# Performance work log

Hardware: AMD Instinct MI355X
Metric: run time of the kernel (lower is better)

## Reference

```python
import jax, jax.numpy as jnp
import numpy as np

SW, FB, EMB, H = 96, 64, 512, 3   # seg_width, freq_bandwidth, embedding_dim, num_heads
B, T = 4, 1024
F = SW * FB


def setup_inputs() -> dict:
    key = jax.random.key(0)
    ks = jax.random.split(key, 12)
    s = 0.02
    dh = SW // H
    return {
        "x": jax.random.normal(ks[0], (B, T, F), jnp.float32),
        "o_enc": jax.random.randint(ks[1], (B, T), 0, 2, jnp.int32),
        "r_enc": jax.random.normal(ks[2], (B, T, EMB), jnp.float32),
        "Wq": jax.random.normal(ks[3], (SW, SW), jnp.float32) * s,
        "bq": jnp.zeros((SW,), jnp.float32),
        "Wk": jax.random.normal(ks[4], (SW, SW), jnp.float32) * s,
        "bk": jnp.zeros((SW,), jnp.float32),
        "Wv": jax.random.normal(ks[5], (SW, SW), jnp.float32) * s,
        "bv": jnp.zeros((SW,), jnp.float32),
        "Er": jax.random.normal(ks[6], (FB, dh), jnp.float32) * s,   # relative pos embeddings, max_len = FB
        "W1": jax.random.normal(ks[7], (SW, 4 * SW), jnp.float32) * s,
        "b1": jnp.zeros((4 * SW,), jnp.float32),
        "W2": jax.random.normal(ks[8], (4 * SW, SW), jnp.float32) * s,
        "b2": jnp.zeros((SW,), jnp.float32),
        "We": jax.random.normal(ks[9], (F, EMB), jnp.float32) * s,
        "be": jnp.zeros((EMB,), jnp.float32),
    }


def _skew(qer):
    # qer: (N, h, L, L) -> Srel via Music-Transformer skewing
    padded = jnp.pad(qer, ((0, 0), (0, 0), (0, 0), (1, 0)))      # (N,h,L,L+1)
    n, h, l, l1 = padded.shape
    return padded.reshape(n, h, l1, l)[:, :, 1:, :]               # (N,h,L,L)


def _rel_attention(x, Wq, bq, Wk, bk, Wv, bv, Er):
    # x: (N, L, D); relative global self-attention with causal mask
    N, L, D = x.shape
    dh = D // H

    def heads(t):
        return t.reshape(N, L, H, dh).transpose(0, 2, 1, 3)       # (N,h,L,dh)

    q = heads(x @ Wq + bq)
    k = heads(x @ Wk + bk)
    v = heads(x @ Wv + bv)
    qer = jnp.einsum('nhld,md->nhlm', q, Er)                      # (N,h,L,L)
    srel = _skew(qer)
    scores = (jnp.einsum('nhld,nhmd->nhlm', q, k) + srel) / jnp.sqrt(jnp.asarray(dh, x.dtype))
    causal = jnp.triu(jnp.ones((L, L), bool), 1)
    scores = jnp.where(causal, jnp.finfo(scores.dtype).min, scores)
    attn = jax.nn.softmax(scores, axis=-1)
    out = jnp.einsum('nhlm,nhmd->nhld', attn, v)
    return out.transpose(0, 2, 1, 3).reshape(N, L, D)


def _segmentwise_mean(data, block_ids):
    # data: (B,T,E), block_ids: (B,T) contiguous non-decreasing segment ids in [0,T)
    Bn, Tn, En = data.shape
    seg_sum = jax.vmap(lambda d, i: jax.ops.segment_sum(d, i, num_segments=Tn))(data, block_ids)
    cnt = jax.vmap(lambda i: jax.ops.segment_sum(jnp.ones_like(i), i, num_segments=Tn))(block_ids)
    means = seg_sum / jnp.maximum(cnt, 1).astype(data.dtype)[..., None]
    is_start = jnp.concatenate(
        [jnp.ones((Bn, 1), bool), block_ids[:, 1:] != block_ids[:, :-1]], axis=1)
    gathered = jnp.take_along_axis(means, block_ids[..., None], axis=1)   # (B,T,E)
    # original writes each block's mean only at the block's first position, zeros elsewhere
    return jnp.where(is_start[..., None], gathered, jnp.zeros((), data.dtype))


def reference(x, o_enc, r_enc, Wq, bq, Wk, bk, Wv, bv, Er, W1, b1, W2, b2, We, be):
    Bn, Tn, Fn = x.shape
    xr = x.reshape(Bn * Tn, SW, FB).transpose(0, 2, 1)            # (B*T, FB, SW)
    emb = _rel_attention(xr, Wq, bq, Wk, bk, Wv, bv, Er)
    emb = jax.nn.relu(emb @ W1 + b1) @ W2 + b2                    # FFN: SW -> 4SW -> SW
    emb = emb.transpose(0, 2, 1).reshape(Bn, Tn, Fn)
    emb = emb @ We + be                                           # (B,T,EMB)
    # nn.LayerNorm(emb.shape): normalize over the WHOLE tensor, no affine, eps=1e-8
    mu = emb.mean()
    var = ((emb - mu) ** 2).mean()
    emb = (emb - mu) / jnp.sqrt(var + 1e-8)
    # _regionalize: block ids from cumsum of binary boundary indicators
    block_ids = jnp.cumsum(o_enc, axis=1)
    block_ids = block_ids - block_ids[:, :1]                      # matches 'if b[0]==1: b -= 1'
    block_means = _segmentwise_mean(emb, block_ids)
    return block_means + r_enc + emb
```

## Files before the change

kernel.cpp:

```cpp
#include <hip/hip_runtime.h>
#include <hip/hip_bf16.h>


typedef __attribute__((ext_vector_type(8))) short bf16x8;
typedef __attribute__((ext_vector_type(4))) float f32x4;

struct PtrTab { const void* p[16]; };

enum : int {
  O_WQT = 0,
  O_BQ  = 9984,
  O_WKT = 10080,
  O_BK  = 20064,
  O_WVT = 20160,
  O_BV  = 30144,
  O_ER  = 30240,
  O_W1T = 32288,
  O_B1  = 72224,
  O_W2C = 72608,
  O_B2  = 118688,
  O_WET = 118784
};

__device__ __forceinline__ float b2f(__hip_bfloat16 v) { return __bfloat162float(v); }
__device__ __forceinline__ __hip_bfloat16 f2b(float v) { return __float2bfloat16(v); }

__global__ __launch_bounds__(256) void prep_kernel(PtrTab tab,
                                                   __hip_bfloat16* __restrict__ Wc,
                                                   float* __restrict__ sums)
{
    __shared__ __hip_bfloat16 tile[64][65];
    const int bid = blockIdx.x, tid = threadIdx.x;
    const int kt = bid % 96, nt = bid / 96;
    const float* We = (const float*)tab.p[14];
    const int k0 = kt * 64, n0 = nt * 64;
    for (int e = tid; e < 4096; e += 256) {
        int kk = e >> 6, nn = e & 63;
        tile[nn][kk] = f2b(We[(size_t)(k0 + kk) * 512 + n0 + nn]);
    }
    __syncthreads();
    __hip_bfloat16* dstT = Wc + O_WET + ((size_t)nt * 96 + kt) * 4096;
    for (int e = tid; e < 4096; e += 256) dstT[e] = tile[e >> 6][e & 63];

    const int g = bid * 256 + tid;
    const int stride = gridDim.x * 256;
    const float* Wq = (const float*)tab.p[3];
    const float* bq = (const float*)tab.p[4];
    const float* Wk = (const float*)tab.p[5];
    const float* bk = (const float*)tab.p[6];
    const float* Wv = (const float*)tab.p[7];
    const float* bv = (const float*)tab.p[8];
    const float* Er = (const float*)tab.p[9];
    const float* W1 = (const float*)tab.p[10];
    const float* b1 = (const float*)tab.p[11];
    const float* W2 = (const float*)tab.p[12];
    const float* b2 = (const float*)tab.p[13];

    for (int t = 0; t < 3; ++t) {
        const float* W = (t == 0 ? Wq : t == 1 ? Wk : Wv);
        __hip_bfloat16* d = Wc + t * 10080;
        for (int i = g; i < 9984; i += stride) {
            int j = i / 104, c = i - j * 104;
            d[i] = (c < 96) ? f2b(W[c * 96 + j]) : f2b(0.0f);
        }
    }
    for (int i = g; i < 96; i += stride) {
        Wc[O_BQ + i] = f2b(bq[i]);
        Wc[O_BK + i] = f2b(bk[i]);
        Wc[O_BV + i] = f2b(bv[i]);
        Wc[O_B2 + i] = f2b(b2[i]);
    }
    for (int i = g; i < 2048; i += stride) Wc[O_ER + i] = f2b(Er[i]);
    for (int i = g; i < 39936; i += stride) {
        int j = i / 104, c = i - j * 104;
        Wc[O_W1T + i] = (c < 96) ? f2b(W1[c * 384 + j]) : f2b(0.0f);
    }
    for (int i = g; i < 384; i += stride) Wc[O_B1 + i] = f2b(b1[i]);
    for (int i = g; i < 46080; i += stride) {
        int kc = i / 3840, r = i - kc * 3840;
        int nn = r / 40, kk = r - nn * 40;
        Wc[O_W2C + i] = (kk < 32) ? f2b(W2[(kc * 32 + kk) * 96 + nn]) : f2b(0.0f);
    }
    if (g < 2) sums[g] = 0.f;
}

__global__ __launch_bounds__(256) void attn_ffn_kernel(
    const float* __restrict__ x, const __hip_bfloat16* __restrict__ Wc,
    __hip_bfloat16* __restrict__ M)
{
    const int n = blockIdx.x, tid = threadIdx.x;
    const int w = tid >> 6, lane = tid & 63, quad = lane >> 4, ln = lane & 15;

    __shared__ __align__(16) char smem[50432];
    __hip_bfloat16* xs  = (__hip_bfloat16*)(smem);
    __hip_bfloat16* wb  = (__hip_bfloat16*)(smem + 13312);
    __hip_bfloat16* PB  = (__hip_bfloat16*)(smem + 13312);
    __hip_bfloat16* kS  = (__hip_bfloat16*)(smem + 23296);
    __hip_bfloat16* vT  = (__hip_bfloat16*)(smem + 36608);
    __hip_bfloat16* hid = (__hip_bfloat16*)(smem + 23296);

    const f32x4 z4 = {0.f, 0.f, 0.f, 0.f};
    const int rowb = 16 * w + quad * 4;

    bf16x8 wf[9], wfn[9];
    #pragma unroll
    for (int i = 0; i < 9; ++i)
        wf[i] = *(const bf16x8*)(Wc + O_WQT + ((i % 3) * 16 + ln) * 104 + (i / 3) * 32 + quad * 8);

    {
        const float* xb = x + (size_t)n * 6144;
        const int sb = w * 24;
        for (int c = 0; c < 3; ++c) {
            float v[8];
            #pragma unroll
            for (int j = 0; j < 8; ++j) v[j] = xb[(sb + c * 8 + j) * 64 + lane];
            union { __hip_bfloat16 h[8]; bf16x8 v8; } pk;
            #pragma unroll
            for (int j = 0; j < 8; ++j) pk.h[j] = f2b(v[j]);
            *(bf16x8*)(xs + lane * 104 + sb + c * 8) = pk.v8;
        }
    }
    __syncthreads();

    bf16x8 aqr[3];

    for (int st = 0; st < 6; ++st) {
        const int t = st >> 1, half = st & 1;
        if (st < 5) {
            const __hip_bfloat16* nb = Wc + ((st + 1) >> 1) * 10080 + ((st + 1) & 1) * 4992;
            #pragma unroll
            for (int i = 0; i < 9; ++i)
                wfn[i] = *(const bf16x8*)(nb + ((i % 3) * 16 + ln) * 104 + (i / 3) * 32 + quad * 8);
        }
        f32x4 acc[3] = {z4, z4, z4};
        #pragma unroll
        for (int ks = 0; ks < 3; ++ks) {
            bf16x8 a = *(const bf16x8*)(xs + (16 * w + ln) * 104 + ks * 32 + quad * 8);
            #pragma unroll
            for (int ct = 0; ct < 3; ++ct)
                acc[ct] = __builtin_amdgcn_mfma_f32_16x16x32_bf16(a, wf[ks * 3 + ct], acc[ct], 0, 0, 0);
        }
        const int j0 = half * 48;
        const __hip_bfloat16* bt = Wc + 9984 + t * 10080;
        #pragma unroll
        for (int ct = 0; ct < 3; ++ct) {
            int col = j0 + ct * 16 + ln;
            float bb = b2f(bt[col]);
            if (t < 2) {
                #pragma unroll
                for (int r = 0; r < 4; ++r)
                    kS[(rowb + r) * 104 + col] = f2b(acc[ct][r] + bb);
            } else {
                union { __hip_bfloat16 h4[4]; uint2 u; } pk;
                #pragma unroll
                for (int r = 0; r < 4; ++r) pk.h4[r] = f2b(acc[ct][r] + bb);
                *(uint2*)(vT + col * 72 + rowb) = pk.u;
            }
        }
        if (t == 0 && half == 1) {
            #pragma unroll
            for (int h = 0; h < 3; ++h)
                aqr[h] = *(const bf16x8*)(kS + (16 * w + ln) * 104 + h * 32 + quad * 8);
        }
        #pragma unroll
        for (int i = 0; i < 9; ++i) wf[i] = wfn[i];
    }

    bf16x8 erf[4];
    #pragma unroll
    for (int tn = 0; tn < 4; ++tn)
        erf[tn] = *(const bf16x8*)(Wc + O_ER + (16 * tn + ln) * 32 + quad * 8);
    __syncthreads();

    bf16x8 pf0, pf1, pf2;
    {
        const bf16x8* src = (const bf16x8*)(Wc + O_W1T);
        pf0 = src[tid]; pf1 = src[tid + 256];
        if (tid + 512 < 624) pf2 = src[tid + 512];
    }

    for (int h = 0; h < 3; ++h) {
        const int c0 = h * 32;
        bf16x8 aq = aqr[h];
        #pragma unroll
        for (int tn = 0; tn < 4; ++tn) {
            f32x4 q4 = __builtin_amdgcn_mfma_f32_16x16x32_bf16(aq, erf[tn], z4, 0, 0, 0);
            #pragma unroll
            for (int r = 0; r < 4; ++r)
                PB[(rowb + r) * 72 + 16 * tn + ln] = f2b(q4[r]);
        }
        float sco[4][4];
        #pragma unroll
        for (int tn = 0; tn < 4; ++tn) {
            bf16x8 kf = *(const bf16x8*)(kS + (16 * tn + ln) * 104 + c0 + quad * 8);
            f32x4 s1 = __builtin_amdgcn_mfma_f32_16x16x32_bf16(aq, kf, z4, 0, 0, 0);
            #pragma unroll
            for (int r = 0; r < 4; ++r) sco[tn][r] = s1[r];
        }
        #pragma unroll
        for (int tn = 0; tn < 4; ++tn)
            #pragma unroll
            for (int r = 0; r < 4; ++r) {
                int row = rowb + r, col = 16 * tn + ln;
                if (col <= row)
                    sco[tn][r] = (sco[tn][r] + b2f(PB[row * 72 + col + 63 - row]))
                                 * 0.17677669529663687f;
                else
                    sco[tn][r] = -3.0e38f;
            }
        float mx[4], sm[4];
        #pragma unroll
        for (int r = 0; r < 4; ++r) {
            float m0 = fmaxf(fmaxf(sco[0][r], sco[1][r]), fmaxf(sco[2][r], sco[3][r]));
            #pragma unroll
            for (int d = 1; d < 16; d <<= 1) m0 = fmaxf(m0, __shfl_xor(m0, d, 64));
            mx[r] = m0;
        }
        #pragma unroll
        for (int tn = 0; tn < 4; ++tn)
            #pragma unroll
            for (int r = 0; r < 4; ++r) sco[tn][r] = __expf(sco[tn][r] - mx[r]);
        #pragma unroll
        for (int r = 0; r < 4; ++r) {
            float s0 = sco[0][r] + sco[1][r] + sco[2][r] + sco[3][r];
            #pragma unroll
            for (int d = 1; d < 16; d <<= 1) s0 += __shfl_xor(s0, d, 64);
            sm[r] = 1.0f / s0;
        }
        #pragma unroll
        for (int tn = 0; tn < 4; ++tn)
            #pragma unroll
            for (int r = 0; r < 4; ++r)
                PB[(rowb + r) * 72 + 16 * tn + ln] = f2b(sco[tn][r] * sm[r]);
        f32x4 oacc[2] = {z4, z4};
        #pragma unroll
        for (int ks2 = 0; ks2 < 2; ++ks2) {
            bf16x8 pa = *(const bf16x8*)(PB + (16 * w + ln) * 72 + ks2 * 32 + quad * 8);
            #pragma unroll
            for (int t2 = 0; t2 < 2; ++t2) {
                bf16x8 vb = *(const bf16x8*)(vT + (c0 + 16 * t2 + ln) * 72 + ks2 * 32 + quad * 8);
                oacc[t2] = __builtin_amdgcn_mfma_f32_16x16x32_bf16(pa, vb, oacc[t2], 0, 0, 0);
            }
        }
        #pragma unroll
        for (int t2 = 0; t2 < 2; ++t2)
            #pragma unroll
            for (int r = 0; r < 4; ++r)
                xs[(rowb + r) * 104 + c0 + 16 * t2 + ln] = f2b(oacc[t2][r]);
    }
    __syncthreads();

    f32x4 acc2[6] = {z4, z4, z4, z4, z4, z4};
    bf16x8 w2f[6], w2fn[6];
    for (int jh = 0; jh < 2; ++jh) {
        for (int cc = 0; cc < 4; ++cc) {
            const int j0g = jh * 192 + cc * 48;
            __syncthreads();
            {
                bf16x8* dst = (bf16x8*)wb;
                dst[tid] = pf0;
                dst[tid + 256] = pf1;
                if (tid + 512 < 624) dst[tid + 512] = pf2;
                if (cc < 3) {
                    const bf16x8* src = (const bf16x8*)(Wc + O_W1T + jh * 19968 + (cc + 1) * 4992);
                    pf0 = src[tid]; pf1 = src[tid + 256];
                    if (tid + 512 < 624) pf2 = src[tid + 512];
                } else {
                    const __hip_bfloat16* nb = Wc + O_W2C + (jh * 6) * 3840;
                    #pragma unroll
                    for (int ct = 0; ct < 6; ++ct)
                        w2f[ct] = *(const bf16x8*)(nb + (ct * 16 + ln) * 40 + quad * 8);
                }
            }
            __syncthreads();
            f32x4 a1[3] = {z4, z4, z4};
            #pragma unroll
            for (int ks = 0; ks < 3; ++ks) {
                bf16x8 a = *(const bf16x8*)(xs + (16 * w + ln) * 104 + ks * 32 + quad * 8);
                #pragma unroll
                for (int ct = 0; ct < 3; ++ct) {
                    bf16x8 b = *(const bf16x8*)(wb + (ct * 16 + ln) * 104 + ks * 32 + quad * 8);
                    a1[ct] = __builtin_amdgcn_mfma_f32_16x16x32_bf16(a, b, a1[ct], 0, 0, 0);
                }
            }
            #pragma unroll
            for (int ct = 0; ct < 3; ++ct) {
                int colg = j0g + ct * 16 + ln;
                int coll = cc * 48 + ct * 16 + ln;
                float bb = b2f(Wc[O_B1 + colg]);
                #pragma unroll
                for (int r = 0; r < 4; ++r)
                    hid[(rowb + r) * 200 + coll] = f2b(fmaxf(a1[ct][r] + bb, 0.f));
            }
        }
        for (int kc = 0; kc < 6; ++kc) {
            if (kc < 5) {
                const __hip_bfloat16* nb = Wc + O_W2C + (jh * 6 + kc + 1) * 3840;
                #pragma unroll
                for (int ct = 0; ct < 6; ++ct)
                    w2fn[ct] = *(const bf16x8*)(nb + (ct * 16 + ln) * 40 + quad * 8);
            } else if (jh == 0) {
                const bf16x8* src = (const bf16x8*)(Wc + O_W1T + 19968);
                pf0 = src[tid]; pf1 = src[tid + 256];
                if (tid + 512 < 624) pf2 = src[tid + 512];
            }
            bf16x8 a = *(const bf16x8*)(hid + (16 * w + ln) * 200 + kc * 32 + quad * 8);
            #pragma unroll
            for (int ct = 0; ct < 6; ++ct)
                acc2[ct] = __builtin_amdgcn_mfma_f32_16x16x32_bf16(a, w2f[ct], acc2[ct], 0, 0, 0);
            if (kc < 5) {
                #pragma unroll
                for (int ct = 0; ct < 6; ++ct) w2f[ct] = w2fn[ct];
            }
        }
    }

    __hip_bfloat16* Mg = M + (size_t)n * 6144;
    #pragma unroll
    for (int ct = 0; ct < 6; ++ct) {
        int d = ct * 16 + ln;
        float bb = b2f(Wc[O_B2 + d]);
        union { __hip_bfloat16 h4[4]; uint2 u; } pk;
        #pragma unroll
        for (int r = 0; r < 4; ++r) pk.h4[r] = f2b(acc2[ct][r] + bb);
        *(uint2*)((char*)Mg + (size_t)(d * 64 + rowb) * 2) = pk.u;
    }
}

__global__ __launch_bounds__(256) void gemm_kernel(
    const __hip_bfloat16* __restrict__ A,
    const __hip_bfloat16* __restrict__ Wc,
    const float* __restrict__ be,
    float* __restrict__ Y,
    float* __restrict__ sums)
{
    __shared__ __align__(16) __hip_bfloat16 As[2][64 * 72];
    __shared__ __align__(16) __hip_bfloat16 Bs[2][64 * 72];
    const int row0 = blockIdx.x * 64, nt = blockIdx.y, col0 = nt * 64;
    const int tid = threadIdx.x;
    const int w = tid >> 6, lane = tid & 63, quad = lane >> 4, ln = lane & 15;
    const int r0 = tid >> 3, c0_ = (tid & 7) * 8;
    const int r1 = r0 + 32,  c1_ = c0_;
    const size_t abase0 = (size_t)(row0 + r0) * 6144 + c0_;
    const size_t abase1 = (size_t)(row0 + r1) * 6144 + c1_;
    const __hip_bfloat16* Bsrc = Wc + O_WET + (size_t)nt * 96 * 4096;
    const size_t bbase0 = (size_t)r0 * 64 + c0_;
    const size_t bbase1 = (size_t)r1 * 64 + c1_;

    const f32x4 z4 = {0.f, 0.f, 0.f, 0.f};
    f32x4 acc[4] = {z4, z4, z4, z4};

    bf16x8 pa0 = *(const bf16x8*)(A + abase0);
    bf16x8 pa1 = *(const bf16x8*)(A + abase1);
    bf16x8 pb0 = *(const bf16x8*)(Bsrc + bbase0);
    bf16x8 pb1 = *(const bf16x8*)(Bsrc + bbase1);
    *(bf16x8*)(&As[0][r0 * 72 + c0_]) = pa0;
    *(bf16x8*)(&As[0][r1 * 72 + c1_]) = pa1;
    *(bf16x8*)(&Bs[0][r0 * 72 + c0_]) = pb0;
    *(bf16x8*)(&Bs[0][r1 * 72 + c1_]) = pb1;
    __syncthreads();

    for (int kt = 0; kt < 96; ++kt) {
        const int cur = kt & 1;
        if (kt < 95) {
            pa0 = *(const bf16x8*)(A + abase0 + (kt + 1) * 64);
            pa1 = *(const bf16x8*)(A + abase1 + (kt + 1) * 64);
            pb0 = *(const bf16x8*)(Bsrc + (size_t)(kt + 1) * 4096 + bbase0);
            pb1 = *(const bf16x8*)(Bsrc + (size_t)(kt + 1) * 4096 + bbase1);
        }
        #pragma unroll
        for (int ks = 0; ks < 2; ++ks) {
            bf16x8 a = *(const bf16x8*)(&As[cur][(16 * w + ln) * 72 + ks * 32 + quad * 8]);
            #pragma unroll
            for (int tn = 0; tn < 4; ++tn) {
                bf16x8 b = *(const bf16x8*)(&Bs[cur][(16 * tn + ln) * 72 + ks * 32 + quad * 8]);
                acc[tn] = __builtin_amdgcn_mfma_f32_16x16x32_bf16(a, b, acc[tn], 0, 0, 0);
            }
        }
        if (kt < 95) {
            *(bf16x8*)(&As[cur ^ 1][r0 * 72 + c0_]) = pa0;
            *(bf16x8*)(&As[cur ^ 1][r1 * 72 + c1_]) = pa1;
            *(bf16x8*)(&Bs[cur ^ 1][r0 * 72 + c0_]) = pb0;
            *(bf16x8*)(&Bs[cur ^ 1][r1 * 72 + c1_]) = pb1;
        }
        __syncthreads();
    }
    float s = 0.f, s2 = 0.f;
    #pragma unroll
    for (int tn = 0; tn < 4; ++tn) {
        int col = col0 + 16 * tn + ln;
        float bb = be[col];
        #pragma unroll
        for (int r = 0; r < 4; ++r) {
            float v = acc[tn][r] + bb;
            Y[(size_t)(row0 + 16 * w + quad * 4 + r) * 512 + col] = v;
            s += v; s2 += v * v;
        }
    }
    #pragma unroll
    for (int off = 1; off < 64; off <<= 1) {
        s  += __shfl_xor(s, off, 64);
        s2 += __shfl_xor(s2, off, 64);
    }
    __shared__ float r1s[4], r2s[4];
    if (lane == 0) { r1s[w] = s; r2s[w] = s2; }
    __syncthreads();
    if (tid == 0) {
        atomicAdd(&sums[0], r1s[0] + r1s[1] + r1s[2] + r1s[3]);
        atomicAdd(&sums[1], r2s[0] + r2s[1] + r2s[2] + r2s[3]);
    }
}

__global__ __launch_bounds__(256) void segid_kernel(const int* __restrict__ o_enc,
                                                    int* __restrict__ bids) {
    __shared__ int ts[256];
    const int b = blockIdx.x, tid = threadIdx.x;
    const int* o = o_enc + b * 1024;
    int v0 = o[4 * tid], v1 = o[4 * tid + 1], v2 = o[4 * tid + 2], v3 = o[4 * tid + 3];
    int p0 = v0, p1 = p0 + v1, p2 = p1 + v2, p3 = p2 + v3;
    ts[tid] = p3;
    __syncthreads();
    for (int off = 1; off < 256; off <<= 1) {
        int mine = ts[tid];
        int add = (tid >= off) ? ts[tid - off] : 0;
        __syncthreads();
        ts[tid] = mine + add;
        __syncthreads();
    }
    const int excl = (tid > 0) ? ts[tid - 1] : 0;
    const int off0 = o[0];
    int* bid = bids + b * 1024;
    bid[4 * tid]     = excl + p0 - off0;
    bid[4 * tid + 1] = excl + p1 - off0;
    bid[4 * tid + 2] = excl + p2 - off0;
    bid[4 * tid + 3] = excl + p3 - off0;
}

__global__ __launch_bounds__(256) void final_kernel(
    const float* __restrict__ Y, const int* __restrict__ bids,
    const float* __restrict__ sums, const float* __restrict__ r_enc,
    float* __restrict__ out)
{
    const int bt = blockIdx.x;
    const int b = bt >> 10, t = bt & 1023;
    const float mu = sums[0] * (1.0f / 2097152.0f);
    const float var = sums[1] * (1.0f / 2097152.0f) - mu * mu;
    const float rstd = rsqrtf(var + 1e-8f);
    const int* bid = bids + b * 1024;
    const int my = bid[t];
    const bool is_start = (t == 0) || (bid[t - 1] != my);
    int t2 = t + 1;
    float invc = 0.f;
    if (is_start) {
        while (t2 < 1024 && bid[t2] == my) ++t2;
        invc = 1.0f / (float)(t2 - t);
    }
    for (int e = threadIdx.x; e < 512; e += 256) {
        const size_t base = (size_t)bt * 512 + e;
        float res = (Y[base] - mu) * rstd + r_enc[base];
        if (is_start) {
            float s = 0.f;
            for (int tt = t; tt < t2; ++tt)
                s += (Y[((size_t)(b * 1024 + tt)) * 512 + e] - mu) * rstd;
            res += s * invc;
        }
        out[base] = res;
    }
}

extern "C" void kernel_launch(void* const* d_in, const int* in_sizes, int n_in,
                              void* d_out, int out_size, void* d_ws, size_t ws_size,
                              hipStream_t stream) {
    PtrTab tab;
    for (int i = 0; i < 16; ++i) tab.p[i] = d_in[i];

    char* ws = (char*)d_ws;
    __hip_bfloat16* M  = (__hip_bfloat16*)ws;
    float* Y           = (float*)(ws + 50331648);
    float* sums        = (float*)(ws + 58720256);
    int*   bids        = (int*)(ws + 58720320);
    __hip_bfloat16* Wc = (__hip_bfloat16*)(ws + 58736768);

    prep_kernel<<<768, 256, 0, stream>>>(tab, Wc, sums);
    attn_ffn_kernel<<<4096, 256, 0, stream>>>((const float*)d_in[0], Wc, M);
    gemm_kernel<<<dim3(64, 8), 256, 0, stream>>>(M, Wc, (const float*)d_in[15], Y, sums);
    segid_kernel<<<4, 256, 0, stream>>>((const int*)d_in[1], bids);
    final_kernel<<<4096, 256, 0, stream>>>(Y, bids, sums, (const float*)d_in[2], (float*)d_out);
}
```

Baseline: 394.3 us.

## Load FFN W1 fragments into registers directly and deepen GEMM prefetch

In the attention+FFN kernel, W1 tiles are no longer staged through shared memory with two barriers per chunk. Each wave now loads its MFMA B fragments straight from global memory into registers, double-buffered one chunk ahead, and the shared buffer shrinks. In the embedding GEMM, global loads are issued two k-steps ahead and the LDS stores for the next tile happen before the MFMAs, so load latency overlaps compute. The cost is more VGPRs (eighteen extra fragment registers), which could lower occupancy, and each wave fetches the W1 data redundantly from global memory or cache.

```diff
diff --git a/kernel.cpp b/kernel.cpp
--- a/kernel.cpp
+++ b/kernel.cpp
@@ -91,13 +91,12 @@
     const int n = blockIdx.x, tid = threadIdx.x;
     const int w = tid >> 6, lane = tid & 63, quad = lane >> 4, ln = lane & 15;
 
-    __shared__ __align__(16) char smem[50432];
+    __shared__ __align__(16) char smem[49664];
     __hip_bfloat16* xs  = (__hip_bfloat16*)(smem);
-    __hip_bfloat16* wb  = (__hip_bfloat16*)(smem + 13312);
     __hip_bfloat16* PB  = (__hip_bfloat16*)(smem + 13312);
-    __hip_bfloat16* kS  = (__hip_bfloat16*)(smem + 23296);
-    __hip_bfloat16* vT  = (__hip_bfloat16*)(smem + 36608);
-    __hip_bfloat16* hid = (__hip_bfloat16*)(smem + 23296);
+    __hip_bfloat16* kS  = (__hip_bfloat16*)(smem + 22528);
+    __hip_bfloat16* vT  = (__hip_bfloat16*)(smem + 35840);
+    __hip_bfloat16* hid = (__hip_bfloat16*)(smem + 22528);
 
     const f32x4 z4 = {0.f, 0.f, 0.f, 0.f};
     const int rowb = 16 * w + quad * 4;
@@ -172,12 +171,10 @@
         erf[tn] = *(const bf16x8*)(Wc + O_ER + (16 * tn + ln) * 32 + quad * 8);
     __syncthreads();
 
-    bf16x8 pf0, pf1, pf2;
-    {
-        const bf16x8* src = (const bf16x8*)(Wc + O_W1T);
-        pf0 = src[tid]; pf1 = src[tid + 256];
-        if (tid + 512 < 624) pf2 = src[tid + 512];
-    }
+    bf16x8 w1f[9], w1fn[9];
+    #pragma unroll
+    for (int i = 0; i < 9; ++i)
+        w1f[i] = *(const bf16x8*)(Wc + O_W1T + ((i % 3) * 16 + ln) * 104 + (i / 3) * 32 + quad * 8);
 
     for (int h = 0; h < 3; ++h) {
         const int c0 = h * 32;
@@ -254,34 +251,26 @@
     bf16x8 w2f[6], w2fn[6];
     for (int jh = 0; jh < 2; ++jh) {
         for (int cc = 0; cc < 4; ++cc) {
-            const int j0g = jh * 192 + cc * 48;
-            __syncthreads();
-            {
-                bf16x8* dst = (bf16x8*)wb;
-                dst[tid] = pf0;
-                dst[tid + 256] = pf1;
-                if (tid + 512 < 624) dst[tid + 512] = pf2;
-                if (cc < 3) {
-                    const bf16x8* src = (const bf16x8*)(Wc + O_W1T + jh * 19968 + (cc + 1) * 4992);
-                    pf0 = src[tid]; pf1 = src[tid + 256];
-                    if (tid + 512 < 624) pf2 = src[tid + 512];
-                } else {
-                    const __hip_bfloat16* nb = Wc + O_W2C + (jh * 6) * 3840;
-                    #pragma unroll
-                    for (int ct = 0; ct < 6; ++ct)
-                        w2f[ct] = *(const bf16x8*)(nb + (ct * 16 + ln) * 40 + quad * 8);
-                }
-            }
-            __syncthreads();
+            const int s = jh * 4 + cc;
+            const int j0g = s * 48;
+            if (cc < 3) {
+                const __hip_bfloat16* nb = Wc + O_W1T + (s + 1) * 4992;
+                #pragma unroll
+                for (int i = 0; i < 9; ++i)
+                    w1fn[i] = *(const bf16x8*)(nb + ((i % 3) * 16 + ln) * 104 + (i / 3) * 32 + quad * 8);
+            } else {
+                const __hip_bfloat16* nb = Wc + O_W2C + (jh * 6) * 3840;
+                #pragma unroll
+                for (int ct = 0; ct < 6; ++ct)
+                    w2f[ct] = *(const bf16x8*)(nb + (ct * 16 + ln) * 40 + quad * 8);
+            }
             f32x4 a1[3] = {z4, z4, z4};
             #pragma unroll
             for (int ks = 0; ks < 3; ++ks) {
                 bf16x8 a = *(const bf16x8*)(xs + (16 * w + ln) * 104 + ks * 32 + quad * 8);
                 #pragma unroll
-                for (int ct = 0; ct < 3; ++ct) {
-                    bf16x8 b = *(const bf16x8*)(wb + (ct * 16 + ln) * 104 + ks * 32 + quad * 8);
-                    a1[ct] = __builtin_amdgcn_mfma_f32_16x16x32_bf16(a, b, a1[ct], 0, 0, 0);
-                }
+                for (int ct = 0; ct < 3; ++ct)
+                    a1[ct] = __builtin_amdgcn_mfma_f32_16x16x32_bf16(a, w1f[ks * 3 + ct], a1[ct], 0, 0, 0);
             }
             #pragma unroll
             for (int ct = 0; ct < 3; ++ct) {
@@ -292,6 +281,10 @@
                 for (int r = 0; r < 4; ++r)
                     hid[(rowb + r) * 200 + coll] = f2b(fmaxf(a1[ct][r] + bb, 0.f));
             }
+            if (cc < 3) {
+                #pragma unroll
+                for (int i = 0; i < 9; ++i) w1f[i] = w1fn[i];
+            }
         }
         for (int kc = 0; kc < 6; ++kc) {
             if (kc < 5) {
@@ -300,9 +293,10 @@
                 for (int ct = 0; ct < 6; ++ct)
                     w2fn[ct] = *(const bf16x8*)(nb + (ct * 16 + ln) * 40 + quad * 8);
             } else if (jh == 0) {
-                const bf16x8* src = (const bf16x8*)(Wc + O_W1T + 19968);
-                pf0 = src[tid]; pf1 = src[tid + 256];
-                if (tid + 512 < 624) pf2 = src[tid + 512];
+                const __hip_bfloat16* nb = Wc + O_W1T + 4 * 4992;
+                #pragma unroll
+                for (int i = 0; i < 9; ++i)
+                    w1f[i] = *(const bf16x8*)(nb + ((i % 3) * 16 + ln) * 104 + (i / 3) * 32 + quad * 8);
             }
             bf16x8 a = *(const bf16x8*)(hid + (16 * w + ln) * 200 + kc * 32 + quad * 8);
             #pragma unroll
@@ -358,30 +352,34 @@
     *(bf16x8*)(&As[0][r1 * 72 + c1_]) = pa1;
     *(bf16x8*)(&Bs[0][r0 * 72 + c0_]) = pb0;
     *(bf16x8*)(&Bs[0][r1 * 72 + c1_]) = pb1;
+    pa0 = *(const bf16x8*)(A + abase0 + 64);
+    pa1 = *(const bf16x8*)(A + abase1 + 64);
+    pb0 = *(const bf16x8*)(Bsrc + 4096 + bbase0);
+    pb1 = *(const bf16x8*)(Bsrc + 4096 + bbase1);
     __syncthreads();
 
     for (int kt = 0; kt < 96; ++kt) {
         const int cur = kt & 1;
-        if (kt < 95) {
-            pa0 = *(const bf16x8*)(A + abase0 + (kt + 1) * 64);
-            pa1 = *(const bf16x8*)(A + abase1 + (kt + 1) * 64);
-            pb0 = *(const bf16x8*)(Bsrc + (size_t)(kt + 1) * 4096 + bbase0);
-            pb1 = *(const bf16x8*)(Bsrc + (size_t)(kt + 1) * 4096 + bbase1);
-        }
-        #pragma unroll
-        for (int ks = 0; ks < 2; ++ks) {
-            bf16x8 a = *(const bf16x8*)(&As[cur][(16 * w + ln) * 72 + ks * 32 + quad * 8]);
-            #pragma unroll
-            for (int tn = 0; tn < 4; ++tn) {
-                bf16x8 b = *(const bf16x8*)(&Bs[cur][(16 * tn + ln) * 72 + ks * 32 + quad * 8]);
-                acc[tn] = __builtin_amdgcn_mfma_f32_16x16x32_bf16(a, b, acc[tn], 0, 0, 0);
-            }
-        }
         if (kt < 95) {
             *(bf16x8*)(&As[cur ^ 1][r0 * 72 + c0_]) = pa0;
             *(bf16x8*)(&As[cur ^ 1][r1 * 72 + c1_]) = pa1;
             *(bf16x8*)(&Bs[cur ^ 1][r0 * 72 + c0_]) = pb0;
             *(bf16x8*)(&Bs[cur ^ 1][r1 * 72 + c1_]) = pb1;
+        }
+        if (kt < 94) {
+            pa0 = *(const bf16x8*)(A + abase0 + (kt + 2) * 64);
+            pa1 = *(const bf16x8*)(A + abase1 + (kt + 2) * 64);
+            pb0 = *(const bf16x8*)(Bsrc + (size_t)(kt + 2) * 4096 + bbase0);
+            pb1 = *(const bf16x8*)(Bsrc + (size_t)(kt + 2) * 4096 + bbase1);
+        }
+        #pragma unroll
+        for (int ks = 0; ks < 2; ++ks) {
+            bf16x8 a = *(const bf16x8*)(&As[cur][(16 * w + ln) * 72 + ks * 32 + quad * 8]);
+            #pragma unroll
+            for (int tn = 0; tn < 4; ++tn) {
+                bf16x8 b = *(const bf16x8*)(&Bs[cur][(16 * tn + ln) * 72 + ks * 32 + quad * 8]);
+                acc[tn] = __builtin_amdgcn_mfma_f32_16x16x32_bf16(a, b, acc[tn], 0, 0, 0);
+            }
         }
         __syncthreads();
     }
```

Result: slower. 431.6 us (+9.5%).
